# Kernel tuning notes

Hardware: AMD Instinct MI355X
Metric: run time of the kernel (lower is better)

The kernel has to match this reference:

```python
import jax, jax.numpy as jnp
import numpy as np


def setup_inputs() -> dict:
    key = jax.random.key(0)
    ks = jax.random.split(key, 5)
    bs, ntok, dm, nh = 4, 256, 64, 4
    x = jax.random.normal(ks[0], (bs, ntok, dm), dtype=jnp.float32)
    wk = jax.random.uniform(ks[1], (nh, dm), dtype=jnp.float32)
    wqv_w = jax.random.normal(ks[2], (3 * nh * dm, dm), dtype=jnp.float32) * 0.02
    wqv_b = jnp.zeros((3 * nh * dm,), dtype=jnp.float32)
    fanin_w = jax.random.normal(ks[3], (dm, dm), dtype=jnp.float32) * 0.02
    fanin_b = jnp.zeros((dm,), dtype=jnp.float32)
    return {"x": x, "wk": wk, "wqv_w": wqv_w, "wqv_b": wqv_b,
            "fanin_w": fanin_w, "fanin_b": fanin_b,
            "layer": 0, "use_dp": 0, "doplot": 0}


def reference(x, wk, wqv_w, wqv_b, fanin_w, fanin_b, layer, use_dp, doplot):
    # L1-attention path (use_dp=False, doplot=False) of ResidualAttentionBlock.forward
    bs, ntok, dm = x.shape
    nh = wk.shape[0]
    delta = 0.2
    # wqv projection -> q, vf, vb each [b, t, nh, dm] (d_head == d_model in this module)
    v = (x @ wqv_w.T + wqv_b).reshape(bs, ntok, 3 * nh, dm)
    q, vf, vb = v[:, :, :nh, :], v[:, :, nh:2 * nh, :], v[:, :, 2 * nh:, :]
    k = x[:, :, None, :] * wk[None, None, :, :]   # [b, s, h, w]
    q = q * wk[None, None, :, :]                   # [b, d, h, w]
    # L1Attn: score[b, s, d, h] = -sum_w |q[b,d,h,w] - k[b,s,h,w]| / sqrt(w);
    # module then negates -> positive scaled L1 distance, applies Huber-like remap, negates back.
    dist = jnp.sum(jnp.abs(q[:, None, :, :, :] - k[:, :, None, :, :]), axis=-1)
    dist = dist / jnp.sqrt(jnp.asarray(dm, dtype=x.dtype))  # [b, s, d, h]
    hub = jnp.where(dist < delta, 0.5 * dist * dist, delta * (dist - 0.5 * delta))
    a = -hub
    af = jax.nn.softmax(a, axis=1)                 # softmax over src tokens
    # (ab = softmax over dst and bb are computed in the original but unused: b = bf)
    bf = jnp.einsum('bsdh,bshw->bdhw', af, vf)     # aggregate values over src
    b = jnp.sum(bf, axis=2)                        # sum over heads -> [b, t, dm]
    y = b * jax.nn.sigmoid(1.702 * b)              # QuickGELU
    y = y @ fanin_w.T + fanin_b
    return x + y
```

## Files before the change

kernel.cpp:

```cpp
#include <hip/hip_runtime.h>

#define BS 4
#define NT 256
#define DM 64
#define NH 4

__global__ __launch_bounds__(256) void k_proj(const float* __restrict__ x,
                                              const float* __restrict__ wk,
                                              const float* __restrict__ wqv_w,
                                              const float* __restrict__ wqv_b,
                                              float* __restrict__ q_s,
                                              float* __restrict__ vf)
{
    __shared__ float xs[8][DM];
    __shared__ float wlds[512][17];

    const int tid  = threadIdx.x;
    const int tok0 = blockIdx.x * 8;

    for (int i = tid; i < 8 * DM; i += 256)
        xs[i >> 6][i & 63] = x[tok0 * DM + i];

    float acc[8][2];
#pragma unroll
    for (int t = 0; t < 8; ++t) { acc[t][0] = 0.f; acc[t][1] = 0.f; }

    const int r = tid;

    for (int cc = 0; cc < 4; ++cc) {
        __syncthreads();
        const int c0 = cc * 16;
        for (int i = tid; i < 512 * 4; i += 256) {
            const int row = i >> 2, c4 = (i & 3) * 4;
            const float4 v = *reinterpret_cast<const float4*>(&wqv_w[row * DM + c0 + c4]);
            wlds[row][c4 + 0] = v.x;
            wlds[row][c4 + 1] = v.y;
            wlds[row][c4 + 2] = v.z;
            wlds[row][c4 + 3] = v.w;
        }
        __syncthreads();
#pragma unroll
        for (int c = 0; c < 16; ++c) {
            const float wa = wlds[r][c];
            const float wb = wlds[r + 256][c];
            const int cg = c0 + c;
#pragma unroll
            for (int t = 0; t < 8; ++t) {
                acc[t][0] += xs[t][cg] * wa;
                acc[t][1] += xs[t][cg] * wb;
            }
        }
    }

    const int h = r >> 6, w = r & 63;
    const float ba  = wqv_b[r];
    const float bb  = wqv_b[r + 256];
    const float wkv = wk[h * DM + w];
#pragma unroll
    for (int t = 0; t < 8; ++t) {
        const int g = tok0 + t;
        const int b = g >> 8, tt = g & 255;
        q_s[(((b * NH) + h) * NT + tt) * DM + w] = (acc[t][0] + ba) * wkv;
        vf [(((b * NH) + h) * NT + tt) * DM + w] =  acc[t][1] + bb;
    }
}

__global__ __launch_bounds__(256) void k_attn(const float* __restrict__ x,
                                              const float* __restrict__ wk,
                                              const float* __restrict__ q_s,
                                              const float* __restrict__ vf,
                                              float* __restrict__ bf)
{
    __shared__ float ks[64][66];
    __shared__ float af_lds[16][NT];
    __shared__ float vfs[64][68];

    const int tid = threadIdx.x;
    const int qt  = blockIdx.x;
    const int bh  = blockIdx.y;
    const int b   = bh >> 2, h = bh & 3;
    const int qg  = tid >> 5;
    const int kg  = tid & 31;

    float q0[DM], q1[DM];
    const float* qbase = q_s + ((b * NH + h) * NT + qt * 16) * DM;
    {
        const float4* p0 = reinterpret_cast<const float4*>(qbase + (qg * 2 + 0) * DM);
        const float4* p1 = reinterpret_cast<const float4*>(qbase + (qg * 2 + 1) * DM);
#pragma unroll
        for (int i = 0; i < 16; ++i) {
            const float4 a = p0[i], c = p1[i];
            q0[4*i+0] = a.x; q0[4*i+1] = a.y; q0[4*i+2] = a.z; q0[4*i+3] = a.w;
            q1[4*i+0] = c.x; q1[4*i+1] = c.y; q1[4*i+2] = c.z; q1[4*i+3] = c.w;
        }
    }

    float dacc[2][8];
#pragma unroll
    for (int j = 0; j < 8; ++j) { dacc[0][j] = 0.f; dacc[1][j] = 0.f; }

    for (int cc = 0; cc < 4; ++cc) {
        __syncthreads();
        {
            const int row = tid >> 2;
            const int c0  = (tid & 3) * 16;
            const float* xp = x + ((b * NT) + cc * 64 + row) * DM + c0;
#pragma unroll
            for (int i = 0; i < 4; ++i) {
                const float4 v  = *reinterpret_cast<const float4*>(xp + i * 4);
                const float4 wv = *reinterpret_cast<const float4*>(wk + h * DM + c0 + i * 4);
                ks[row][c0 + i*4 + 0] = v.x * wv.x;
                ks[row][c0 + i*4 + 1] = v.y * wv.y;
                ks[row][c0 + i*4 + 2] = v.z * wv.z;
                ks[row][c0 + i*4 + 3] = v.w * wv.w;
            }
        }
        __syncthreads();
#pragma unroll
        for (int k2 = 0; k2 < 2; ++k2) {
            const int kr = kg + 32 * k2;
            float d0 = 0.f, d1 = 0.f;
#pragma unroll
            for (int c = 0; c < 64; ++c) {
                const float kv = ks[kr][c];
                d0 += fabsf(q0[c] - kv);
                d1 += fabsf(q1[c] - kv);
            }
            dacc[0][cc * 2 + k2] = d0;
            dacc[1][cc * 2 + k2] = d1;
        }
    }

    const float delta = 0.2f;
    float aa[2][8];
    float m0 = -1e30f, m1 = -1e30f;
#pragma unroll
    for (int j = 0; j < 8; ++j) {
        float d = dacc[0][j] * 0.125f;
        float hb = (d < delta) ? 0.5f * d * d : delta * (d - 0.5f * delta);
        aa[0][j] = -hb; m0 = fmaxf(m0, -hb);
        d = dacc[1][j] * 0.125f;
        hb = (d < delta) ? 0.5f * d * d : delta * (d - 0.5f * delta);
        aa[1][j] = -hb; m1 = fmaxf(m1, -hb);
    }
#pragma unroll
    for (int mask = 1; mask < 32; mask <<= 1) {
        m0 = fmaxf(m0, __shfl_xor(m0, mask, 32));
        m1 = fmaxf(m1, __shfl_xor(m1, mask, 32));
    }
    float s0 = 0.f, s1 = 0.f;
#pragma unroll
    for (int j = 0; j < 8; ++j) {
        aa[0][j] = __expf(aa[0][j] - m0); s0 += aa[0][j];
        aa[1][j] = __expf(aa[1][j] - m1); s1 += aa[1][j];
    }
#pragma unroll
    for (int mask = 1; mask < 32; mask <<= 1) {
        s0 += __shfl_xor(s0, mask, 32);
        s1 += __shfl_xor(s1, mask, 32);
    }
    const float rs0 = 1.f / s0, rs1 = 1.f / s1;
#pragma unroll
    for (int j = 0; j < 8; ++j) {
        const int cc = j >> 1, k2 = j & 1;
        const int skey = cc * 64 + kg + 32 * k2;
        af_lds[qg * 2 + 0][skey] = aa[0][j] * rs0;
        af_lds[qg * 2 + 1][skey] = aa[1][j] * rs1;
    }

    const int qi = tid >> 4;
    const int wg = tid & 15;
    float4 acc = make_float4(0.f, 0.f, 0.f, 0.f);

    for (int cc = 0; cc < 4; ++cc) {
        __syncthreads();
        {
            const int row = tid >> 2;
            const int c0  = (tid & 3) * 16;
            const float* vp = vf + ((b * NH + h) * NT + cc * 64 + row) * DM + c0;
#pragma unroll
            for (int i = 0; i < 4; ++i) {
                const float4 v = *reinterpret_cast<const float4*>(vp + i * 4);
                *reinterpret_cast<float4*>(&vfs[row][c0 + i * 4]) = v;
            }
        }
        __syncthreads();
#pragma unroll
        for (int s = 0; s < 64; ++s) {
            const float a = af_lds[qi][cc * 64 + s];
            const float4 v = *reinterpret_cast<const float4*>(&vfs[s][wg * 4]);
            acc.x += a * v.x; acc.y += a * v.y; acc.z += a * v.z; acc.w += a * v.w;
        }
    }
    float* op = bf + ((b * NH + h) * NT + qt * 16 + qi) * DM + wg * 4;
    *reinterpret_cast<float4*>(op) = acc;
}

__global__ __launch_bounds__(256) void k_out(const float* __restrict__ x,
                                             const float* __restrict__ bf,
                                             const float* __restrict__ fanin_w,
                                             const float* __restrict__ fanin_b,
                                             float* __restrict__ out)
{
    __shared__ float fw[64][65];
    __shared__ float ys[16][64];

    const int tid  = threadIdx.x;
    const int tok0 = blockIdx.x * 16;

    for (int i = tid * 4; i < 4096; i += 1024) {
        const float4 v = *reinterpret_cast<const float4*>(fanin_w + i);
        const int row = i >> 6, c = i & 63;
        fw[row][c + 0] = v.x; fw[row][c + 1] = v.y;
        fw[row][c + 2] = v.z; fw[row][c + 3] = v.w;
    }
    for (int idx = tid; idx < 16 * 64; idx += 256) {
        const int t = idx >> 6, c = idx & 63;
        const int g = tok0 + t, b = g >> 8, tt = g & 255;
        float s = 0.f;
#pragma unroll
        for (int h = 0; h < NH; ++h)
            s += bf[((b * NH + h) * NT + tt) * DM + c];
        ys[t][c] = s * (1.f / (1.f + __expf(-1.702f * s)));
    }
    __syncthreads();
    for (int idx = tid; idx < 16 * 64; idx += 256) {
        const int t = idx >> 6, w = idx & 63;
        float acc = fanin_b[w];
#pragma unroll
        for (int c = 0; c < 64; ++c)
            acc += ys[t][c] * fw[w][c];
        const int g = tok0 + t;
        out[g * DM + w] = x[g * DM + w] + acc;
    }
}

extern "C" void kernel_launch(void* const* d_in, const int* in_sizes, int n_in,
                              void* d_out, int out_size, void* d_ws, size_t ws_size,
                              hipStream_t stream) {
    const float* x       = (const float*)d_in[0];
    const float* wk      = (const float*)d_in[1];
    const float* wqv_w   = (const float*)d_in[2];
    const float* wqv_b   = (const float*)d_in[3];
    const float* fanin_w = (const float*)d_in[4];
    const float* fanin_b = (const float*)d_in[5];
    float* out = (float*)d_out;

    float* ws  = (float*)d_ws;
    float* q_s = ws;
    float* vfw = ws + 262144;
    float* bfw = ws + 524288;

    hipLaunchKernelGGL(k_proj, dim3(128),     dim3(256), 0, stream,
                       x, wk, wqv_w, wqv_b, q_s, vfw);
    hipLaunchKernelGGL(k_attn, dim3(16, 16),  dim3(256), 0, stream,
                       x, wk, q_s, vfw, bfw);
    hipLaunchKernelGGL(k_out,  dim3(64),      dim3(256), 0, stream,
                       x, bfw, fanin_w, fanin_b, out);
}
```

Measured before the change: 106.1 us.

## Restructure all three kernels for more blocks, direct weight reads, split-K AV

k_proj now handles 4 tokens per block and reads weight rows directly from global memory as float4 instead of staging them through LDS, and it launches twice as many blocks. k_attn loads the whole V tile into LDS once. Its AV product is split across four source-range groups, each accumulating four query rows, followed by an LDS reduction, which removes the per-chunk sync loop. k_out uses 4 tokens per block with 256 blocks and vectorised float4 dot products. The aim is more parallelism and fewer barriers, at the cost of more LDS per attention block (about 86KB), which may limit occupancy.

Measured after the change: 100.8 us. -5.0%, faster.

```diff
diff --git a/kernel.cpp b/kernel.cpp
--- a/kernel.cpp
+++ b/kernel.cpp
@@ -1,6 +1,5 @@
 #include <hip/hip_runtime.h>
 
-#define BS 4
 #define NT 256
 #define DM 64
 #define NH 4
@@ -12,58 +11,47 @@
                                               float* __restrict__ q_s,
                                               float* __restrict__ vf)
 {
-    __shared__ float xs[8][DM];
-    __shared__ float wlds[512][17];
-
+    __shared__ float xs[4 * DM];
     const int tid  = threadIdx.x;
-    const int tok0 = blockIdx.x * 8;
-
-    for (int i = tid; i < 8 * DM; i += 256)
-        xs[i >> 6][i & 63] = x[tok0 * DM + i];
-
-    float acc[8][2];
-#pragma unroll
-    for (int t = 0; t < 8; ++t) { acc[t][0] = 0.f; acc[t][1] = 0.f; }
-
-    const int r = tid;
-
-    for (int cc = 0; cc < 4; ++cc) {
-        __syncthreads();
-        const int c0 = cc * 16;
-        for (int i = tid; i < 512 * 4; i += 256) {
-            const int row = i >> 2, c4 = (i & 3) * 4;
-            const float4 v = *reinterpret_cast<const float4*>(&wqv_w[row * DM + c0 + c4]);
-            wlds[row][c4 + 0] = v.x;
-            wlds[row][c4 + 1] = v.y;
-            wlds[row][c4 + 2] = v.z;
-            wlds[row][c4 + 3] = v.w;
-        }
-        __syncthreads();
-#pragma unroll
-        for (int c = 0; c < 16; ++c) {
-            const float wa = wlds[r][c];
-            const float wb = wlds[r + 256][c];
-            const int cg = c0 + c;
-#pragma unroll
-            for (int t = 0; t < 8; ++t) {
-                acc[t][0] += xs[t][cg] * wa;
-                acc[t][1] += xs[t][cg] * wb;
-            }
-        }
-    }
-
-    const int h = r >> 6, w = r & 63;
-    const float ba  = wqv_b[r];
-    const float bb  = wqv_b[r + 256];
-    const float wkv = wk[h * DM + w];
-#pragma unroll
-    for (int t = 0; t < 8; ++t) {
-        const int g = tok0 + t;
-        const int b = g >> 8, tt = g & 255;
-        q_s[(((b * NH) + h) * NT + tt) * DM + w] = (acc[t][0] + ba) * wkv;
-        vf [(((b * NH) + h) * NT + tt) * DM + w] =  acc[t][1] + bb;
-    }
-}
+    const int tok0 = blockIdx.x * 4;
+
+    if (tid < 64)
+        reinterpret_cast<float4*>(xs)[tid] =
+            reinterpret_cast<const float4*>(x + tok0 * DM)[tid];
+    __syncthreads();
+
+    const float4* wr0 = reinterpret_cast<const float4*>(wqv_w + tid * DM);
+    const float4* wr1 = reinterpret_cast<const float4*>(wqv_w + (tid + 256) * DM);
+    float a0[4] = {0.f, 0.f, 0.f, 0.f};
+    float a1[4] = {0.f, 0.f, 0.f, 0.f};
+
+#pragma unroll
+    for (int c4 = 0; c4 < 16; ++c4) {
+        const float4 wa = wr0[c4];
+        const float4 wb = wr1[c4];
+#pragma unroll
+        for (int t = 0; t < 4; ++t) {
+            const float4 xv = reinterpret_cast<const float4*>(xs + t * DM)[c4];
+            a0[t] += xv.x * wa.x + xv.y * wa.y + xv.z * wa.z + xv.w * wa.w;
+            a1[t] += xv.x * wb.x + xv.y * wb.y + xv.z * wb.z + xv.w * wb.w;
+        }
+    }
+
+    const int h = tid >> 6, w = tid & 63;
+    const float ba = wqv_b[tid];
+    const float bb = wqv_b[tid + 256];
+    const float kw = wk[h * DM + w];
+#pragma unroll
+    for (int t = 0; t < 4; ++t) {
+        const int g = tok0 + t, b = g >> 8, tt = g & 255;
+        const int o = ((b * NH + h) * NT + tt) * DM + w;
+        q_s[o] = (a0[t] + ba) * kw;
+        vf[o]  =  a1[t] + bb;
+    }
+}
+
+#define KS_LD 66
+#define AF_LD 258
 
 __global__ __launch_bounds__(256) void k_attn(const float* __restrict__ x,
                                               const float* __restrict__ wk,
@@ -71,9 +59,10 @@
                                               const float* __restrict__ vf,
                                               float* __restrict__ bf)
 {
-    __shared__ float ks[64][66];
-    __shared__ float af_lds[16][NT];
-    __shared__ float vfs[64][68];
+    __shared__ float ks[64 * KS_LD];
+    __shared__ float af[16 * AF_LD];
+    __shared__ float vfs[NT * DM];
+    __shared__ float part[4 * 16 * DM];
 
     const int tid = threadIdx.x;
     const int qt  = blockIdx.x;
@@ -83,17 +72,20 @@
     const int kg  = tid & 31;
 
     float q0[DM], q1[DM];
-    const float* qbase = q_s + ((b * NH + h) * NT + qt * 16) * DM;
-    {
-        const float4* p0 = reinterpret_cast<const float4*>(qbase + (qg * 2 + 0) * DM);
-        const float4* p1 = reinterpret_cast<const float4*>(qbase + (qg * 2 + 1) * DM);
+    {
+        const float4* p0 = reinterpret_cast<const float4*>(
+            q_s + ((b * NH + h) * NT + qt * 16 + qg * 2) * DM);
+        const float4* p1 = p0 + 16;
 #pragma unroll
         for (int i = 0; i < 16; ++i) {
-            const float4 a = p0[i], c = p1[i];
-            q0[4*i+0] = a.x; q0[4*i+1] = a.y; q0[4*i+2] = a.z; q0[4*i+3] = a.w;
-            q1[4*i+0] = c.x; q1[4*i+1] = c.y; q1[4*i+2] = c.z; q1[4*i+3] = c.w;
-        }
-    }
+            const float4 u = p0[i];
+            q0[4*i] = u.x; q0[4*i+1] = u.y; q0[4*i+2] = u.z; q0[4*i+3] = u.w;
+            const float4 v = p1[i];
+            q1[4*i] = v.x; q1[4*i+1] = v.y; q1[4*i+2] = v.z; q1[4*i+3] = v.w;
+        }
+    }
+
+    const float4* wkr = reinterpret_cast<const float4*>(wk + h * DM);
 
     float dacc[2][8];
 #pragma unroll
@@ -102,46 +94,54 @@
     for (int cc = 0; cc < 4; ++cc) {
         __syncthreads();
         {
-            const int row = tid >> 2;
-            const int c0  = (tid & 3) * 16;
-            const float* xp = x + ((b * NT) + cc * 64 + row) * DM + c0;
+            const int row = tid >> 2, c0 = (tid & 3) * 16;
+            const float4* xp = reinterpret_cast<const float4*>(
+                x + ((b * NT) + cc * 64 + row) * DM + c0);
+            float* kp = ks + row * KS_LD + c0;
 #pragma unroll
             for (int i = 0; i < 4; ++i) {
-                const float4 v  = *reinterpret_cast<const float4*>(xp + i * 4);
-                const float4 wv = *reinterpret_cast<const float4*>(wk + h * DM + c0 + i * 4);
-                ks[row][c0 + i*4 + 0] = v.x * wv.x;
-                ks[row][c0 + i*4 + 1] = v.y * wv.y;
-                ks[row][c0 + i*4 + 2] = v.z * wv.z;
-                ks[row][c0 + i*4 + 3] = v.w * wv.w;
+                const float4 v  = xp[i];
+                const float4 wv = wkr[(c0 >> 2) + i];
+                reinterpret_cast<float2*>(kp)[2*i]     = make_float2(v.x * wv.x, v.y * wv.y);
+                reinterpret_cast<float2*>(kp)[2*i + 1] = make_float2(v.z * wv.z, v.w * wv.w);
             }
         }
         __syncthreads();
 #pragma unroll
         for (int k2 = 0; k2 < 2; ++k2) {
-            const int kr = kg + 32 * k2;
+            const float2* kp = reinterpret_cast<const float2*>(ks + (kg + 32 * k2) * KS_LD);
             float d0 = 0.f, d1 = 0.f;
 #pragma unroll
-            for (int c = 0; c < 64; ++c) {
-                const float kv = ks[kr][c];
-                d0 += fabsf(q0[c] - kv);
-                d1 += fabsf(q1[c] - kv);
+            for (int c2 = 0; c2 < 32; ++c2) {
+                const float2 kv = kp[c2];
+                d0 += fabsf(q0[2*c2] - kv.x) + fabsf(q0[2*c2+1] - kv.y);
+                d1 += fabsf(q1[2*c2] - kv.x) + fabsf(q1[2*c2+1] - kv.y);
             }
             dacc[0][cc * 2 + k2] = d0;
             dacc[1][cc * 2 + k2] = d1;
         }
     }
 
+    {
+        const float4* vp = reinterpret_cast<const float4*>(vf + (b * NH + h) * NT * DM);
+#pragma unroll
+        for (int it = 0; it < 16; ++it) {
+            const int qidx = it * 256 + tid;
+            reinterpret_cast<float4*>(vfs)[qidx] = vp[qidx];
+        }
+    }
+
     const float delta = 0.2f;
-    float aa[2][8];
+    float aa0[8], aa1[8];
     float m0 = -1e30f, m1 = -1e30f;
 #pragma unroll
     for (int j = 0; j < 8; ++j) {
-        float d = dacc[0][j] * 0.125f;
+        float d  = dacc[0][j] * 0.125f;
         float hb = (d < delta) ? 0.5f * d * d : delta * (d - 0.5f * delta);
-        aa[0][j] = -hb; m0 = fmaxf(m0, -hb);
-        d = dacc[1][j] * 0.125f;
+        aa0[j] = -hb; m0 = fmaxf(m0, aa0[j]);
+        d  = dacc[1][j] * 0.125f;
         hb = (d < delta) ? 0.5f * d * d : delta * (d - 0.5f * delta);
-        aa[1][j] = -hb; m1 = fmaxf(m1, -hb);
+        aa1[j] = -hb; m1 = fmaxf(m1, aa1[j]);
     }
 #pragma unroll
     for (int mask = 1; mask < 32; mask <<= 1) {
@@ -151,8 +151,8 @@
     float s0 = 0.f, s1 = 0.f;
 #pragma unroll
     for (int j = 0; j < 8; ++j) {
-        aa[0][j] = __expf(aa[0][j] - m0); s0 += aa[0][j];
-        aa[1][j] = __expf(aa[1][j] - m1); s1 += aa[1][j];
+        aa0[j] = __expf(aa0[j] - m0); s0 += aa0[j];
+        aa1[j] = __expf(aa1[j] - m1); s1 += aa1[j];
     }
 #pragma unroll
     for (int mask = 1; mask < 32; mask <<= 1) {
@@ -162,38 +162,54 @@
     const float rs0 = 1.f / s0, rs1 = 1.f / s1;
 #pragma unroll
     for (int j = 0; j < 8; ++j) {
-        const int cc = j >> 1, k2 = j & 1;
-        const int skey = cc * 64 + kg + 32 * k2;
-        af_lds[qg * 2 + 0][skey] = aa[0][j] * rs0;
-        af_lds[qg * 2 + 1][skey] = aa[1][j] * rs1;
-    }
-
-    const int qi = tid >> 4;
-    const int wg = tid & 15;
-    float4 acc = make_float4(0.f, 0.f, 0.f, 0.f);
-
-    for (int cc = 0; cc < 4; ++cc) {
-        __syncthreads();
-        {
-            const int row = tid >> 2;
-            const int c0  = (tid & 3) * 16;
-            const float* vp = vf + ((b * NH + h) * NT + cc * 64 + row) * DM + c0;
-#pragma unroll
-            for (int i = 0; i < 4; ++i) {
-                const float4 v = *reinterpret_cast<const float4*>(vp + i * 4);
-                *reinterpret_cast<float4*>(&vfs[row][c0 + i * 4]) = v;
-            }
-        }
-        __syncthreads();
+        const int skey = (j >> 1) * 64 + (j & 1) * 32 + kg;
+        af[(qg * 2 + 0) * AF_LD + skey] = aa0[j] * rs0;
+        af[(qg * 2 + 1) * AF_LD + skey] = aa1[j] * rs1;
+    }
+    __syncthreads();
+
+    {
+        const int wq  = tid & 15;
+        const int qg4 = (tid >> 4) & 3;
+        const int sr  = tid >> 6;
+
+        float4 acc0 = {0,0,0,0}, acc1 = {0,0,0,0}, acc2 = {0,0,0,0}, acc3 = {0,0,0,0};
+        const float* afb = af + (qg4 * 4) * AF_LD + sr * 64;
+        const float* vb  = vfs + (sr * 64) * DM + wq * 4;
 #pragma unroll
         for (int s = 0; s < 64; ++s) {
-            const float a = af_lds[qi][cc * 64 + s];
-            const float4 v = *reinterpret_cast<const float4*>(&vfs[s][wg * 4]);
-            acc.x += a * v.x; acc.y += a * v.y; acc.z += a * v.z; acc.w += a * v.w;
-        }
-    }
-    float* op = bf + ((b * NH + h) * NT + qt * 16 + qi) * DM + wg * 4;
-    *reinterpret_cast<float4*>(op) = acc;
+            const float4 v = *reinterpret_cast<const float4*>(vb + s * DM);
+            const float a0 = afb[0 * AF_LD + s];
+            const float a1 = afb[1 * AF_LD + s];
+            const float a2 = afb[2 * AF_LD + s];
+            const float a3 = afb[3 * AF_LD + s];
+            acc0.x += a0 * v.x; acc0.y += a0 * v.y; acc0.z += a0 * v.z; acc0.w += a0 * v.w;
+            acc1.x += a1 * v.x; acc1.y += a1 * v.y; acc1.z += a1 * v.z; acc1.w += a1 * v.w;
+            acc2.x += a2 * v.x; acc2.y += a2 * v.y; acc2.z += a2 * v.z; acc2.w += a2 * v.w;
+            acc3.x += a3 * v.x; acc3.y += a3 * v.y; acc3.z += a3 * v.z; acc3.w += a3 * v.w;
+        }
+        float* pp = part + (sr * 16 + qg4 * 4) * DM + wq * 4;
+        *reinterpret_cast<float4*>(pp + 0 * DM) = acc0;
+        *reinterpret_cast<float4*>(pp + 1 * DM) = acc1;
+        *reinterpret_cast<float4*>(pp + 2 * DM) = acc2;
+        *reinterpret_cast<float4*>(pp + 3 * DM) = acc3;
+    }
+    __syncthreads();
+
+    {
+        const int q = tid >> 4, w4 = tid & 15;
+        const float* pp = part + q * DM + w4 * 4;
+        float4 r0 = *reinterpret_cast<const float4*>(pp);
+        const float4 r1 = *reinterpret_cast<const float4*>(pp + 16 * DM);
+        const float4 r2 = *reinterpret_cast<const float4*>(pp + 32 * DM);
+        const float4 r3 = *reinterpret_cast<const float4*>(pp + 48 * DM);
+        r0.x += r1.x + r2.x + r3.x;
+        r0.y += r1.y + r2.y + r3.y;
+        r0.z += r1.z + r2.z + r3.z;
+        r0.w += r1.w + r2.w + r3.w;
+        float* op = bf + ((b * NH + h) * NT + qt * 16 + q) * DM + w4 * 4;
+        *reinterpret_cast<float4*>(op) = r0;
+    }
 }
 
 __global__ __launch_bounds__(256) void k_out(const float* __restrict__ x,
@@ -202,34 +218,40 @@
                                              const float* __restrict__ fanin_b,
                                              float* __restrict__ out)
 {
-    __shared__ float fw[64][65];
-    __shared__ float ys[16][64];
+    __shared__ float fw[64 * 68];
+    __shared__ float ys[4 * DM];
 
     const int tid  = threadIdx.x;
-    const int tok0 = blockIdx.x * 16;
-
-    for (int i = tid * 4; i < 4096; i += 1024) {
-        const float4 v = *reinterpret_cast<const float4*>(fanin_w + i);
-        const int row = i >> 6, c = i & 63;
-        fw[row][c + 0] = v.x; fw[row][c + 1] = v.y;
-        fw[row][c + 2] = v.z; fw[row][c + 3] = v.w;
-    }
-    for (int idx = tid; idx < 16 * 64; idx += 256) {
-        const int t = idx >> 6, c = idx & 63;
+    const int tok0 = blockIdx.x * 4;
+
+#pragma unroll
+    for (int it = 0; it < 4; ++it) {
+        const int qidx = it * 256 + tid;
+        const int row = qidx >> 4, cq = qidx & 15;
+        *reinterpret_cast<float4*>(fw + row * 68 + cq * 4) =
+            reinterpret_cast<const float4*>(fanin_w)[qidx];
+    }
+    {
+        const int t = tid >> 6, c = tid & 63;
         const int g = tok0 + t, b = g >> 8, tt = g & 255;
         float s = 0.f;
 #pragma unroll
-        for (int h = 0; h < NH; ++h)
-            s += bf[((b * NH + h) * NT + tt) * DM + c];
-        ys[t][c] = s * (1.f / (1.f + __expf(-1.702f * s)));
-    }
-    __syncthreads();
-    for (int idx = tid; idx < 16 * 64; idx += 256) {
-        const int t = idx >> 6, w = idx & 63;
+        for (int hh = 0; hh < NH; ++hh)
+            s += bf[((b * NH + hh) * NT + tt) * DM + c];
+        ys[t * DM + c] = s / (1.f + __expf(-1.702f * s));
+    }
+    __syncthreads();
+    {
+        const int t = tid >> 6, w = tid & 63;
         float acc = fanin_b[w];
-#pragma unroll
-        for (int c = 0; c < 64; ++c)
-            acc += ys[t][c] * fw[w][c];
+        const float* yr = ys + t * DM;
+        const float* fr = fw + w * 68;
+#pragma unroll
+        for (int c4 = 0; c4 < 16; ++c4) {
+            const float4 yv = *reinterpret_cast<const float4*>(yr + c4 * 4);
+            const float4 fv = *reinterpret_cast<const float4*>(fr + c4 * 4);
+            acc += yv.x * fv.x + yv.y * fv.y + yv.z * fv.z + yv.w * fv.w;
+        }
         const int g = tok0 + t;
         out[g * DM + w] = x[g * DM + w] + acc;
     }
@@ -251,10 +273,10 @@
     float* vfw = ws + 262144;
     float* bfw = ws + 524288;
 
-    hipLaunchKernelGGL(k_proj, dim3(128),     dim3(256), 0, stream,
+    hipLaunchKernelGGL(k_proj, dim3(256),     dim3(256), 0, stream,
                        x, wk, wqv_w, wqv_b, q_s, vfw);
     hipLaunchKernelGGL(k_attn, dim3(16, 16),  dim3(256), 0, stream,
                        x, wk, q_s, vfw, bfw);
-    hipLaunchKernelGGL(k_out,  dim3(64),      dim3(256), 0, stream,
+    hipLaunchKernelGGL(k_out,  dim3(256),     dim3(256), 0, stream,
                        x, bfw, fanin_w, fanin_b, out);
 }
```
